# Optimization experiments

Hardware: AMD Instinct MI355X
Metric: run time of the kernel (lower is better)

## Reference

```python
import jax, jax.numpy as jnp
import numpy as np

B, G, K, C, NT = 128, 64, 32, 256, 8192


def setup_inputs() -> dict:
    key = jax.random.key(0)
    ks = jax.random.split(key, 8)
    s = lambda fan_in: 1.0 / np.sqrt(fan_in)
    return {
        "patch_features": jax.random.normal(ks[0], (B, G, C), jnp.float32),
        "neighborhood": jax.random.normal(ks[1], (B, G, K, 3), jnp.float32),
        "codebook": jax.random.normal(ks[2], (NT, C), jnp.float32),
        "w1": jax.random.normal(ks[3], (512, C), jnp.float32) * s(C),
        "b1": jnp.zeros((512,), jnp.float32),
        "w2": jax.random.normal(ks[4], (256, 512), jnp.float32) * s(512),
        "b2": jnp.zeros((256,), jnp.float32),
        "w3": jax.random.normal(ks[5], (3 * K, 256), jnp.float32) * s(256),
        "b3": jnp.zeros((3 * K,), jnp.float32),
    }


def reference(patch_features, neighborhood, codebook, w1, b1, w2, b2, w3, b3):
    b, g, c = patch_features.shape
    k = neighborhood.shape[2]
    # squared euclidean distances to codebook (argmin equals argmin of cdist p=2)
    d2 = (
        jnp.sum(patch_features * patch_features, -1, keepdims=True)
        - 2.0 * jnp.einsum("bgc,nc->bgn", patch_features, codebook)
        + jnp.sum(codebook * codebook, -1)
    )  # [B,G,NT]
    token_ids = jnp.argmin(d2, axis=-1)          # [B,G]
    quantized = codebook[token_ids]              # [B,G,C] gather
    # 1x1 Conv1d stack == per-token MLP
    h = jax.nn.relu(jnp.einsum("bgc,oc->bgo", quantized, w1) + b1)
    h = jax.nn.relu(jnp.einsum("bgc,oc->bgo", h, w2) + b2)
    rec = jnp.einsum("bgc,oc->bgo", h, w3) + b3  # [B,G,3K]
    rec = rec.reshape(b * g, k, 3)
    gt = neighborhood.reshape(b * g, k, 3)
    # Chamfer distance L2 (squared) both directions
    diff = rec[:, :, None, :] - gt[:, None, :, :]  # [BG,K,K,3]
    dd = jnp.sum(diff * diff, -1)                  # [BG,K,K]
    loss = jnp.mean(jnp.min(dd, axis=2)) + jnp.mean(jnp.min(dd, axis=1))
    return loss
```

## Files before the change

### kernel.cpp

```cpp
#include <hip/hip_runtime.h>
#include <hip/hip_bf16.h>
#include <float.h>

#define NTOK 8192
#define NCB  8192
#define CDIM 256
#define KPTS 32
#define SQNT 24.0f
#define INV_CFOLD (SQNT * SQNT * 64.0f)

typedef __attribute__((ext_vector_type(8))) short short8;
typedef __attribute__((ext_vector_type(4))) float f32x4;
typedef __attribute__((ext_vector_type(4))) int i32x4;
typedef unsigned int u32;
typedef unsigned long long u64;

__device__ __forceinline__ void gl_lds16(const void* g, void* l) {
  __builtin_amdgcn_global_load_lds(
      (const __attribute__((address_space(1))) u32*)(g),
      (__attribute__((address_space(3))) u32*)(l), 16, 0, 0);
}

__device__ __forceinline__ ushort bf16_rne(float x) {
  u32 u = __float_as_uint(x);
  return (ushort)((u + 0x7fffu + ((u >> 16) & 1u)) >> 16);
}

__device__ __forceinline__ int pack4i8(int a, int b, int c, int d) {
  return (a & 0xff) | ((b & 0xff) << 8) | ((c & 0xff) << 16) | ((d & 0xff) << 24);
}

__global__ __launch_bounds__(256) void prep_k(
    const float* __restrict__ pf, const float* __restrict__ cb,
    const float* __restrict__ w1, const float* __restrict__ w2,
    const float* __restrict__ w3,
    i32x4* __restrict__ pf1, i32x4* __restrict__ pf2,
    i32x4* __restrict__ cb1, i32x4* __restrict__ cb2,
    ushort* __restrict__ cb_bf, ushort* __restrict__ w1s,
    ushort* __restrict__ w2s, ushort* __restrict__ w3s,
    float* __restrict__ cnorm) {
  int gid = blockIdx.x * 4 + (threadIdx.x >> 6);
  int lane = threadIdx.x & 63, r16 = lane & 15, quad = lane >> 4;
  if (gid < 4096) {
    bool is_cb = gid >= 2048;
    int t = is_cb ? gid - 2048 : gid;
    int tile = t >> 2, kb = t & 3;
    const float* src = is_cb ? cb : pf;
    int row = tile * 16 + r16;
    const float* sp = src + (size_t)row * CDIM + kb * 64 + quad * 16;
    float4 v0 = ((const float4*)sp)[0];
    float4 v1 = ((const float4*)sp)[1];
    float4 v2 = ((const float4*)sp)[2];
    float4 v3 = ((const float4*)sp)[3];
    float x[16] = {v0.x, v0.y, v0.z, v0.w, v1.x, v1.y, v1.z, v1.w,
                   v2.x, v2.y, v2.z, v2.w, v3.x, v3.y, v3.z, v3.w};
    int q1[16], q2[16];
    float s = 0.f;
#pragma unroll
    for (int e = 0; e < 16; e++) {
      float as = x[e] * SQNT;
      float a1 = rintf(as);
      a1 = fminf(fmaxf(a1, -127.f), 127.f);
      float a2 = rintf((as - a1) * 128.f);
      a2 = fminf(fmaxf(a2, -127.f), 127.f);
      q1[e] = (int)a1;
      q2[e] = (int)a2;
      s += x[e] * x[e];
    }
    i32x4 p1 = {pack4i8(q1[0], q1[1], q1[2], q1[3]),
                pack4i8(q1[4], q1[5], q1[6], q1[7]),
                pack4i8(q1[8], q1[9], q1[10], q1[11]),
                pack4i8(q1[12], q1[13], q1[14], q1[15])};
    i32x4 p2 = {pack4i8(q2[0], q2[1], q2[2], q2[3]),
                pack4i8(q2[4], q2[5], q2[6], q2[7]),
                pack4i8(q2[8], q2[9], q2[10], q2[11]),
                pack4i8(q2[12], q2[13], q2[14], q2[15])};
    size_t o = (size_t)t * 64 + lane;
    (is_cb ? cb1 : pf1)[o] = p1;
    (is_cb ? cb2 : pf2)[o] = p2;
    if (is_cb) {
      s += __shfl_xor(s, 16, 64);
      s += __shfl_xor(s, 32, 64);
      if (quad == 0) atomicAdd(cnorm + row, s);
    }
  } else if (gid < 8192) {
    int t = gid - 4096;
    int tile = t >> 3, kb = t & 7;
    int row = tile * 16 + r16;
    const float* sp = cb + (size_t)row * CDIM + kb * 32 + quad * 8;
    float4 a = ((const float4*)sp)[0];
    float4 b = ((const float4*)sp)[1];
    short8 vh = {(short)bf16_rne(a.x), (short)bf16_rne(a.y),
                 (short)bf16_rne(a.z), (short)bf16_rne(a.w),
                 (short)bf16_rne(b.x), (short)bf16_rne(b.y),
                 (short)bf16_rne(b.z), (short)bf16_rne(b.w)};
    *(short8*)(cb_bf + ((size_t)tile * 8 + kb) * 512 + lane * 8) = vh;
  } else if (gid < 8752) {
    int t = gid - 8192;
    const float* src;
    ushort* dst;
    int KB;
    if (t < 256)      { src = w1; dst = w1s; KB = 8; }
    else if (t < 512) { src = w2; dst = w2s; KB = 16; t -= 256; }
    else              { src = w3; dst = w3s; KB = 8;  t -= 512; }
    int tile = t / KB, kb = t - tile * KB, K = KB * 32;
    int row = tile * 16 + r16;
    const float* sp = src + (size_t)row * K + kb * 32 + quad * 8;
    float4 a = ((const float4*)sp)[0];
    float4 b = ((const float4*)sp)[1];
    short8 vh = {(short)bf16_rne(a.x), (short)bf16_rne(a.y),
                 (short)bf16_rne(a.z), (short)bf16_rne(a.w),
                 (short)bf16_rne(b.x), (short)bf16_rne(b.y),
                 (short)bf16_rne(b.z), (short)bf16_rne(b.w)};
    *(short8*)(dst + ((size_t)tile * KB + kb) * 512 + lane * 8) = vh;
  }
}

__global__ __launch_bounds__(256, 2) void argmin_k(
    const char* __restrict__ A1g, const char* __restrict__ A2g,
    const char* __restrict__ B1g, const char* __restrict__ B2g,
    const float* __restrict__ cnorm, u64* __restrict__ pkeys) {
  __shared__ char lds[2][32768];
  int tid = threadIdx.x;
  int ns = blockIdx.x, mt = blockIdx.y;
  int wv = tid >> 6, lane = tid & 63;
  int quad = lane >> 4, r16 = lane & 15;
  int wr = wv >> 1, wc = wv & 1;

  int bvi[4][4], bii[4][4];
#pragma unroll
  for (int i = 0; i < 4; i++)
#pragma unroll
    for (int r = 0; r < 4; r++) { bvi[i][r] = 0x7fffffff; bii[i][r] = 0x7fffffff; }

  const char* bsrc = (wv == 0) ? A1g : (wv == 1) ? A2g : (wv == 2) ? B1g : B2g;

  i32x4 am[4][4], ac[4][4];

  auto stage = [&](int s) {
    int nts = s >> 2, kb = s & 3;
    int nt = ns * 4 + nts;
    char* dst = lds[s & 1] + wv * 8192;
    int gt0 = ((wv < 2) ? mt : nt) * 8;
#pragma unroll
    for (int u = 0; u < 8; ++u)
      gl_lds16(bsrc + ((size_t)(gt0 + u) * 4 + kb) * 1024 + lane * 16,
               dst + u * 1024);
  };

  stage(0);
  __syncthreads();
  for (int s = 0; s < 16; ++s) {
    int kb = s & 3, nts = s >> 2;
    if (kb == 0) {
#pragma unroll
      for (int i = 0; i < 4; i++)
#pragma unroll
        for (int j = 0; j < 4; j++) {
          am[i][j] = (i32x4){0, 0, 0, 0};
          ac[i][j] = (i32x4){0, 0, 0, 0};
        }
    }
    if (s < 15) stage(s + 1);
    const char* L = lds[s & 1];
    i32x4 f1[4], f2[4], g1[4], g2[4];
#pragma unroll
    for (int i = 0; i < 4; i++) {
      f1[i] = *(const i32x4*)(L + (wr * 4 + i) * 1024 + lane * 16);
      f2[i] = *(const i32x4*)(L + (8 + wr * 4 + i) * 1024 + lane * 16);
    }
#pragma unroll
    for (int j = 0; j < 4; j++) {
      g1[j] = *(const i32x4*)(L + (16 + wc * 4 + j) * 1024 + lane * 16);
      g2[j] = *(const i32x4*)(L + (24 + wc * 4 + j) * 1024 + lane * 16);
    }
#pragma unroll
    for (int i = 0; i < 4; i++)
#pragma unroll
      for (int j = 0; j < 4; j++) {
        am[i][j] = __builtin_amdgcn_mfma_i32_16x16x64_i8(f1[i], g1[j], am[i][j], 0, 0, 0);
        ac[i][j] = __builtin_amdgcn_mfma_i32_16x16x64_i8(f1[i], g2[j], ac[i][j], 0, 0, 0);
        ac[i][j] = __builtin_amdgcn_mfma_i32_16x16x64_i8(f2[i], g1[j], ac[i][j], 0, 0, 0);
      }
    if (kb == 3) {
      int nt = ns * 4 + nts;
#pragma unroll
      for (int j = 0; j < 4; j++) {
        int col = nt * 128 + wc * 64 + j * 16 + r16;
        int cni = __float2int_rn(cnorm[col] * INV_CFOLD);
#pragma unroll
        for (int i = 0; i < 4; i++)
#pragma unroll
          for (int r = 0; r < 4; r++) {
            int di = cni - (am[i][j][r] * 128 + ac[i][j][r]);
            if (di < bvi[i][r]) { bvi[i][r] = di; bii[i][r] = col; }
          }
      }
    }
    __syncthreads();
  }
#pragma unroll
  for (int m = 1; m < 16; m <<= 1) {
#pragma unroll
    for (int i = 0; i < 4; i++)
#pragma unroll
      for (int r = 0; r < 4; r++) {
        int ov = __shfl_xor(bvi[i][r], m, 64);
        int oi = __shfl_xor(bii[i][r], m, 64);
        if (ov < bvi[i][r] || (ov == bvi[i][r] && oi < bii[i][r])) {
          bvi[i][r] = ov;
          bii[i][r] = oi;
        }
      }
  }
  if (r16 == 0) {
#pragma unroll
    for (int i = 0; i < 4; i++)
#pragma unroll
      for (int r = 0; r < 4; r++) {
        int row = mt * 128 + wr * 64 + i * 16 + quad * 4 + r;
        u32 mk = (u32)(bvi[i][r] + (1 << 30));
        pkeys[(size_t)(ns * 2 + wc) * NTOK + row] = ((u64)mk << 32) | (u32)bii[i][r];
      }
  }
}

__global__ __launch_bounds__(512) void mlp_fused_k(
    const u64* __restrict__ pkeys, const ushort* __restrict__ cb_bf,
    const ushort* __restrict__ w1s, const float* __restrict__ b1,
    const ushort* __restrict__ w2s, const float* __restrict__ b2,
    const ushort* __restrict__ w3s, const float* __restrict__ b3,
    const float* __restrict__ neigh, float* __restrict__ out) {
  __shared__ ushort qs_h2[8 * 512];
  __shared__ ushort h1s[16 * 512];
  __shared__ float rec[16 * 96];
  __shared__ float gts[16 * 96];
  __shared__ int ids[16];
  __shared__ float wsum[8];

  int tid = threadIdx.x;
  int t0 = blockIdx.x * 16;
  int wv = tid >> 6, lane = tid & 63;
  int quad = lane >> 4, r16 = lane & 15;

  {
    int row_l = tid >> 5, sl = tid & 31;
    u64 best = pkeys[(size_t)sl * NTOK + t0 + row_l];
#pragma unroll
    for (int m = 1; m < 32; m <<= 1) {
      u64 o = __shfl_xor((unsigned long long)best, m, 64);
      if (o < best) best = o;
    }
    if (sl == 0) ids[row_l] = (int)(u32)best;
  }
  __syncthreads();

  {
    int kb = wv;
    int id = ids[r16];
    short8 v = *(const short8*)(cb_bf + ((size_t)(id >> 4) * 8 + kb) * 512 +
                                (size_t)((id & 15) + quad * 16) * 8);
    *(short8*)(qs_h2 + (size_t)kb * 512 + lane * 8) = v;
  }
  __syncthreads();

  short8 fa1[8];
#pragma unroll
  for (int kb = 0; kb < 8; kb++)
    fa1[kb] = *(const short8*)(qs_h2 + (size_t)kb * 512 + lane * 8);
  __syncthreads();

#pragma unroll
  for (int jj = 0; jj < 4; ++jj) {
    int jt = wv + jj * 8;
    f32x4 acc = (f32x4){0.f, 0.f, 0.f, 0.f};
#pragma unroll
    for (int kb = 0; kb < 8; kb++) {
      short8 fb = *(const short8*)(w1s + ((size_t)jt * 8 + kb) * 512 + lane * 8);
      acc = __builtin_amdgcn_mfma_f32_16x16x32_bf16(fa1[kb], fb, acc, 0, 0, 0);
    }
    int col = jt * 16 + r16;
    float bj = b1[col];
#pragma unroll
    for (int reg = 0; reg < 4; reg++) {
      int row_l = quad * 4 + reg;
      float v = fmaxf(acc[reg] + bj, 0.f);
      size_t o = (size_t)(col >> 5) * 512 +
                 (size_t)(((col >> 3) & 3) * 16 + row_l) * 8 + (col & 7);
      h1s[o] = bf16_rne(v);
    }
  }
  __syncthreads();

#pragma unroll
  for (int jj = 0; jj < 2; ++jj) {
    int jt = wv + jj * 8;
    f32x4 acc = (f32x4){0.f, 0.f, 0.f, 0.f};
#pragma unroll
    for (int kb = 0; kb < 16; kb++) {
      short8 fa = *(const short8*)(h1s + (size_t)kb * 512 + lane * 8);
      short8 fb = *(const short8*)(w2s + ((size_t)jt * 16 + kb) * 512 + lane * 8);
      acc = __builtin_amdgcn_mfma_f32_16x16x32_bf16(fa, fb, acc, 0, 0, 0);
    }
    int col = jt * 16 + r16;
    float bj = b2[col];
#pragma unroll
    for (int reg = 0; reg < 4; reg++) {
      int row_l = quad * 4 + reg;
      float v = fmaxf(acc[reg] + bj, 0.f);
      size_t o = (size_t)(col >> 5) * 512 +
                 (size_t)(((col >> 3) & 3) * 16 + row_l) * 8 + (col & 7);
      qs_h2[o] = bf16_rne(v);
    }
  }
  __syncthreads();

  if (tid < 384) {
    int t = tid / 24, c = (tid - t * 24) * 4;
    *(float4*)(gts + (size_t)t * 96 + c) =
        *(const float4*)(neigh + (size_t)(t0 + t) * 96 + c);
  }

  if (wv < 6) {
    int jt = wv;
    f32x4 acc = (f32x4){0.f, 0.f, 0.f, 0.f};
#pragma unroll
    for (int kb = 0; kb < 8; kb++) {
      short8 fa = *(const short8*)(qs_h2 + (size_t)kb * 512 + lane * 8);
      short8 fb = *(const short8*)(w3s + ((size_t)jt * 8 + kb) * 512 + lane * 8);
      acc = __builtin_amdgcn_mfma_f32_16x16x32_bf16(fa, fb, acc, 0, 0, 0);
    }
    int col = jt * 16 + r16;
    float bj = b3[col];
#pragma unroll
    for (int reg = 0; reg < 4; reg++) {
      int row_l = quad * 4 + reg;
      rec[(size_t)row_l * 96 + col] = acc[reg] + bj;
    }
  }
  __syncthreads();

  float local = 0.f;
  {
    int t = tid >> 5, i = tid & 31;
    float rx = rec[t * 96 + 3 * i], ry = rec[t * 96 + 3 * i + 1], rz = rec[t * 96 + 3 * i + 2];
    float gx = gts[t * 96 + 3 * i], gy = gts[t * 96 + 3 * i + 1], gz = gts[t * 96 + 3 * i + 2];
    float mA = FLT_MAX, mB = FLT_MAX;
#pragma unroll
    for (int j = 0; j < 32; j++) {
      float dx = rx - gts[t * 96 + 3 * j], dy = ry - gts[t * 96 + 3 * j + 1],
            dz = rz - gts[t * 96 + 3 * j + 2];
      float d = dx * dx + dy * dy + dz * dz;
      mA = fminf(mA, d);
      dx = rec[t * 96 + 3 * j] - gx; dy = rec[t * 96 + 3 * j + 1] - gy;
      dz = rec[t * 96 + 3 * j + 2] - gz;
      d = dx * dx + dy * dy + dz * dz;
      mB = fminf(mB, d);
    }
    local = mA + mB;
  }
#pragma unroll
  for (int off = 32; off; off >>= 1) local += __shfl_down(local, off, 64);
  if (lane == 0) wsum[wv] = local;
  __syncthreads();
  if (tid == 0) {
    float s = 0.f;
#pragma unroll
    for (int w = 0; w < 8; w++) s += wsum[w];
    atomicAdd(out, s * (1.0f / (float)(NTOK * KPTS)));
  }
}

extern "C" void kernel_launch(void* const* d_in, const int* in_sizes, int n_in,
                              void* d_out, int out_size, void* d_ws, size_t ws_size,
                              hipStream_t stream) {
  const float* pf    = (const float*)d_in[0];
  const float* neigh = (const float*)d_in[1];
  const float* cb    = (const float*)d_in[2];
  const float* w1    = (const float*)d_in[3];
  const float* b1    = (const float*)d_in[4];
  const float* w2    = (const float*)d_in[5];
  const float* b2    = (const float*)d_in[6];
  const float* w3    = (const float*)d_in[7];
  const float* b3    = (const float*)d_in[8];
  float* out = (float*)d_out;
  char* base = (char*)d_ws;

  u64*   pkeys = (u64*)base;
  float* cnorm = (float*)(base + 0x200000);
  char*  pf1   = base + 0x210000;
  char*  pf2   = base + 0x410000;
  char*  cb1   = base + 0x610000;
  char*  cb2   = base + 0x810000;
  ushort* cb_bf = (ushort*)(base + 0xA10000);
  ushort* w1s   = (ushort*)(base + 0xE10000);
  ushort* w2s   = (ushort*)(base + 0xE50000);
  ushort* w3s   = (ushort*)(base + 0xE90000);

  hipMemsetAsync(d_out, 0, sizeof(float), stream);
  hipMemsetAsync(cnorm, 0, NCB * sizeof(float), stream);
  prep_k<<<2188, 256, 0, stream>>>(pf, cb, w1, w2, w3,
                                   (i32x4*)pf1, (i32x4*)pf2, (i32x4*)cb1,
                                   (i32x4*)cb2, cb_bf, w1s, w2s, w3s, cnorm);
  argmin_k<<<dim3(16, 64), 256, 0, stream>>>(pf1, pf2, cb1, cb2, cnorm, pkeys);
  mlp_fused_k<<<512, 512, 0, stream>>>(pkeys, cb_bf, w1s, b1, w2s, b2,
                                       w3s, b3, neigh, out);
}
```

Measured before the change: 167.0 us.

## Retile argmin and MLP kernels, fuse codebook bf16 conversion and norm reduction

Prep now writes the bf16 codebook from the same loads used for int8 quantization and reduces codebook norms in shared memory instead of with atomics, which drops a memset and about half the prep blocks. The argmin kernel shrinks its M tile to 64 rows, uses a single 24KB LDS buffer and targets 3 blocks per CU. This trades the double-buffered prefetch for more occupancy and smaller register footprint. The MLP kernel processes 32 tokens per block so each weight fragment load feeds two MFMAs.

```diff
diff --git a/kernel.cpp b/kernel.cpp
--- a/kernel.cpp
+++ b/kernel.cpp
@@ -39,7 +39,9 @@
     ushort* __restrict__ cb_bf, ushort* __restrict__ w1s,
     ushort* __restrict__ w2s, ushort* __restrict__ w3s,
     float* __restrict__ cnorm) {
+  __shared__ float cred[4][16];
   int gid = blockIdx.x * 4 + (threadIdx.x >> 6);
+  int wv = threadIdx.x >> 6;
   int lane = threadIdx.x & 63, r16 = lane & 15, quad = lane >> 4;
   if (gid < 4096) {
     bool is_cb = gid >= 2048;
@@ -79,24 +81,33 @@
     (is_cb ? cb1 : pf1)[o] = p1;
     (is_cb ? cb2 : pf2)[o] = p2;
     if (is_cb) {
+      int kb32 = 2 * kb + (quad >> 1);
+      int slot0 = ((2 * quad) & 3) * 16 + r16;
+      int slot1 = ((2 * quad + 1) & 3) * 16 + r16;
+      size_t bo = ((size_t)tile * 8 + kb32) * 512;
+      short8 vh0 = {(short)bf16_rne(x[0]), (short)bf16_rne(x[1]),
+                    (short)bf16_rne(x[2]), (short)bf16_rne(x[3]),
+                    (short)bf16_rne(x[4]), (short)bf16_rne(x[5]),
+                    (short)bf16_rne(x[6]), (short)bf16_rne(x[7])};
+      short8 vh1 = {(short)bf16_rne(x[8]), (short)bf16_rne(x[9]),
+                    (short)bf16_rne(x[10]), (short)bf16_rne(x[11]),
+                    (short)bf16_rne(x[12]), (short)bf16_rne(x[13]),
+                    (short)bf16_rne(x[14]), (short)bf16_rne(x[15])};
+      *(short8*)(cb_bf + bo + (size_t)slot0 * 8) = vh0;
+      *(short8*)(cb_bf + bo + (size_t)slot1 * 8) = vh1;
       s += __shfl_xor(s, 16, 64);
       s += __shfl_xor(s, 32, 64);
-      if (quad == 0) atomicAdd(cnorm + row, s);
-    }
-  } else if (gid < 8192) {
+      if (quad == 0) cred[wv][r16] = s;
+      __syncthreads();
+      if (threadIdx.x < 16) {
+        int ctile = blockIdx.x - 512;
+        cnorm[ctile * 16 + threadIdx.x] =
+            cred[0][threadIdx.x] + cred[1][threadIdx.x] +
+            cred[2][threadIdx.x] + cred[3][threadIdx.x];
+      }
+    }
+  } else if (gid < 4656) {
     int t = gid - 4096;
-    int tile = t >> 3, kb = t & 7;
-    int row = tile * 16 + r16;
-    const float* sp = cb + (size_t)row * CDIM + kb * 32 + quad * 8;
-    float4 a = ((const float4*)sp)[0];
-    float4 b = ((const float4*)sp)[1];
-    short8 vh = {(short)bf16_rne(a.x), (short)bf16_rne(a.y),
-                 (short)bf16_rne(a.z), (short)bf16_rne(a.w),
-                 (short)bf16_rne(b.x), (short)bf16_rne(b.y),
-                 (short)bf16_rne(b.z), (short)bf16_rne(b.w)};
-    *(short8*)(cb_bf + ((size_t)tile * 8 + kb) * 512 + lane * 8) = vh;
-  } else if (gid < 8752) {
-    int t = gid - 8192;
     const float* src;
     ushort* dst;
     int KB;
@@ -116,80 +127,73 @@
   }
 }
 
-__global__ __launch_bounds__(256, 2) void argmin_k(
+__global__ __launch_bounds__(256, 3) void argmin_k(
     const char* __restrict__ A1g, const char* __restrict__ A2g,
     const char* __restrict__ B1g, const char* __restrict__ B2g,
     const float* __restrict__ cnorm, u64* __restrict__ pkeys) {
-  __shared__ char lds[2][32768];
+  __shared__ char lds[24 * 1024];
   int tid = threadIdx.x;
   int ns = blockIdx.x, mt = blockIdx.y;
   int wv = tid >> 6, lane = tid & 63;
   int quad = lane >> 4, r16 = lane & 15;
   int wr = wv >> 1, wc = wv & 1;
 
-  int bvi[4][4], bii[4][4];
-#pragma unroll
-  for (int i = 0; i < 4; i++)
+  int bvi[2][4], bii[2][4];
+#pragma unroll
+  for (int i = 0; i < 2; i++)
 #pragma unroll
     for (int r = 0; r < 4; r++) { bvi[i][r] = 0x7fffffff; bii[i][r] = 0x7fffffff; }
 
-  const char* bsrc = (wv == 0) ? A1g : (wv == 1) ? A2g : (wv == 2) ? B1g : B2g;
-
-  i32x4 am[4][4], ac[4][4];
-
-  auto stage = [&](int s) {
+  i32x4 am[2][4], ac[2][4];
+
+  for (int s = 0; s < 16; ++s) {
     int nts = s >> 2, kb = s & 3;
     int nt = ns * 4 + nts;
-    char* dst = lds[s & 1] + wv * 8192;
-    int gt0 = ((wv < 2) ? mt : nt) * 8;
-#pragma unroll
-    for (int u = 0; u < 8; ++u)
-      gl_lds16(bsrc + ((size_t)(gt0 + u) * 4 + kb) * 1024 + lane * 16,
-               dst + u * 1024);
-  };
-
-  stage(0);
-  __syncthreads();
-  for (int s = 0; s < 16; ++s) {
-    int kb = s & 3, nts = s >> 2;
+#pragma unroll
+    for (int u = 0; u < 6; ++u) {
+      int c = wv + u * 4;
+      const char* src;
+      int gt;
+      if (c < 4)       { src = A1g; gt = mt * 4 + c; }
+      else if (c < 8)  { src = A2g; gt = mt * 4 + (c - 4); }
+      else if (c < 16) { src = B1g; gt = nt * 8 + (c - 8); }
+      else             { src = B2g; gt = nt * 8 + (c - 16); }
+      gl_lds16(src + ((size_t)gt * 4 + kb) * 1024 + lane * 16, lds + c * 1024);
+    }
+    __syncthreads();
     if (kb == 0) {
 #pragma unroll
-      for (int i = 0; i < 4; i++)
+      for (int i = 0; i < 2; i++)
 #pragma unroll
         for (int j = 0; j < 4; j++) {
           am[i][j] = (i32x4){0, 0, 0, 0};
           ac[i][j] = (i32x4){0, 0, 0, 0};
         }
     }
-    if (s < 15) stage(s + 1);
-    const char* L = lds[s & 1];
-    i32x4 f1[4], f2[4], g1[4], g2[4];
-#pragma unroll
-    for (int i = 0; i < 4; i++) {
-      f1[i] = *(const i32x4*)(L + (wr * 4 + i) * 1024 + lane * 16);
-      f2[i] = *(const i32x4*)(L + (8 + wr * 4 + i) * 1024 + lane * 16);
+    i32x4 f1[2], f2[2];
+#pragma unroll
+    for (int i = 0; i < 2; i++) {
+      f1[i] = *(const i32x4*)(lds + (wr * 2 + i) * 1024 + lane * 16);
+      f2[i] = *(const i32x4*)(lds + 4096 + (wr * 2 + i) * 1024 + lane * 16);
     }
 #pragma unroll
     for (int j = 0; j < 4; j++) {
-      g1[j] = *(const i32x4*)(L + (16 + wc * 4 + j) * 1024 + lane * 16);
-      g2[j] = *(const i32x4*)(L + (24 + wc * 4 + j) * 1024 + lane * 16);
-    }
-#pragma unroll
-    for (int i = 0; i < 4; i++)
-#pragma unroll
-      for (int j = 0; j < 4; j++) {
-        am[i][j] = __builtin_amdgcn_mfma_i32_16x16x64_i8(f1[i], g1[j], am[i][j], 0, 0, 0);
-        ac[i][j] = __builtin_amdgcn_mfma_i32_16x16x64_i8(f1[i], g2[j], ac[i][j], 0, 0, 0);
-        ac[i][j] = __builtin_amdgcn_mfma_i32_16x16x64_i8(f2[i], g1[j], ac[i][j], 0, 0, 0);
-      }
+      i32x4 g1 = *(const i32x4*)(lds + 8192 + (wc * 4 + j) * 1024 + lane * 16);
+      i32x4 g2 = *(const i32x4*)(lds + 16384 + (wc * 4 + j) * 1024 + lane * 16);
+#pragma unroll
+      for (int i = 0; i < 2; i++) {
+        am[i][j] = __builtin_amdgcn_mfma_i32_16x16x64_i8(f1[i], g1, am[i][j], 0, 0, 0);
+        ac[i][j] = __builtin_amdgcn_mfma_i32_16x16x64_i8(f1[i], g2, ac[i][j], 0, 0, 0);
+        ac[i][j] = __builtin_amdgcn_mfma_i32_16x16x64_i8(f2[i], g1, ac[i][j], 0, 0, 0);
+      }
+    }
     if (kb == 3) {
-      int nt = ns * 4 + nts;
 #pragma unroll
       for (int j = 0; j < 4; j++) {
         int col = nt * 128 + wc * 64 + j * 16 + r16;
         int cni = __float2int_rn(cnorm[col] * INV_CFOLD);
 #pragma unroll
-        for (int i = 0; i < 4; i++)
+        for (int i = 0; i < 2; i++)
 #pragma unroll
           for (int r = 0; r < 4; r++) {
             int di = cni - (am[i][j][r] * 128 + ac[i][j][r]);
@@ -202,7 +206,7 @@
 #pragma unroll
   for (int m = 1; m < 16; m <<= 1) {
 #pragma unroll
-    for (int i = 0; i < 4; i++)
+    for (int i = 0; i < 2; i++)
 #pragma unroll
       for (int r = 0; r < 4; r++) {
         int ov = __shfl_xor(bvi[i][r], m, 64);
@@ -215,10 +219,10 @@
   }
   if (r16 == 0) {
 #pragma unroll
-    for (int i = 0; i < 4; i++)
+    for (int i = 0; i < 2; i++)
 #pragma unroll
       for (int r = 0; r < 4; r++) {
-        int row = mt * 128 + wr * 64 + i * 16 + quad * 4 + r;
+        int row = mt * 64 + wr * 32 + i * 16 + quad * 4 + r;
         u32 mk = (u32)(bvi[i][r] + (1 << 30));
         pkeys[(size_t)(ns * 2 + wc) * NTOK + row] = ((u64)mk << 32) | (u32)bii[i][r];
       }
@@ -231,23 +235,26 @@
     const ushort* __restrict__ w2s, const float* __restrict__ b2,
     const ushort* __restrict__ w3s, const float* __restrict__ b3,
     const float* __restrict__ neigh, float* __restrict__ out) {
-  __shared__ ushort qs_h2[8 * 512];
-  __shared__ ushort h1s[16 * 512];
-  __shared__ float rec[16 * 96];
-  __shared__ float gts[16 * 96];
-  __shared__ int ids[16];
-  __shared__ float wsum[8];
+  extern __shared__ char lds[];
+  ushort* qsp = (ushort*)lds;
+  ushort* h1p = (ushort*)(lds + 16384);
+  float* recp = (float*)(lds + 16384);
+  float* gtsp = (float*)(lds + 28672);
+  int* ids = (int*)(lds + 49152);
+  float* wsum = (float*)(lds + 49280);
 
   int tid = threadIdx.x;
-  int t0 = blockIdx.x * 16;
+  int t0 = blockIdx.x * 32;
   int wv = tid >> 6, lane = tid & 63;
   int quad = lane >> 4, r16 = lane & 15;
 
   {
-    int row_l = tid >> 5, sl = tid & 31;
-    u64 best = pkeys[(size_t)sl * NTOK + t0 + row_l];
-#pragma unroll
-    for (int m = 1; m < 32; m <<= 1) {
+    int row_l = tid >> 4, sl = tid & 15;
+    u64 a = pkeys[(size_t)sl * NTOK + t0 + row_l];
+    u64 b = pkeys[(size_t)(sl + 16) * NTOK + t0 + row_l];
+    u64 best = a < b ? a : b;
+#pragma unroll
+    for (int m = 1; m < 16; m <<= 1) {
       u64 o = __shfl_xor((unsigned long long)best, m, 64);
       if (o < best) best = o;
     }
@@ -255,39 +262,46 @@
   }
   __syncthreads();
 
-  {
-    int kb = wv;
-    int id = ids[r16];
-    short8 v = *(const short8*)(cb_bf + ((size_t)(id >> 4) * 8 + kb) * 512 +
+#pragma unroll
+  for (int t = 0; t < 2; t++) {
+    int id = ids[t * 16 + r16];
+    short8 v = *(const short8*)(cb_bf + ((size_t)(id >> 4) * 8 + wv) * 512 +
                                 (size_t)((id & 15) + quad * 16) * 8);
-    *(short8*)(qs_h2 + (size_t)kb * 512 + lane * 8) = v;
-  }
-  __syncthreads();
-
-  short8 fa1[8];
-#pragma unroll
-  for (int kb = 0; kb < 8; kb++)
-    fa1[kb] = *(const short8*)(qs_h2 + (size_t)kb * 512 + lane * 8);
-  __syncthreads();
+    *(short8*)(qsp + (size_t)(t * 8 + wv) * 512 + lane * 8) = v;
+  }
+  __syncthreads();
+
+  short8 fa1[2][8];
+#pragma unroll
+  for (int t = 0; t < 2; t++)
+#pragma unroll
+    for (int kb = 0; kb < 8; kb++)
+      fa1[t][kb] = *(const short8*)(qsp + (size_t)(t * 8 + kb) * 512 + lane * 8);
 
 #pragma unroll
   for (int jj = 0; jj < 4; ++jj) {
     int jt = wv + jj * 8;
-    f32x4 acc = (f32x4){0.f, 0.f, 0.f, 0.f};
+    f32x4 acc0 = (f32x4){0.f, 0.f, 0.f, 0.f};
+    f32x4 acc1 = (f32x4){0.f, 0.f, 0.f, 0.f};
 #pragma unroll
     for (int kb = 0; kb < 8; kb++) {
       short8 fb = *(const short8*)(w1s + ((size_t)jt * 8 + kb) * 512 + lane * 8);
-      acc = __builtin_amdgcn_mfma_f32_16x16x32_bf16(fa1[kb], fb, acc, 0, 0, 0);
+      acc0 = __builtin_amdgcn_mfma_f32_16x16x32_bf16(fa1[0][kb], fb, acc0, 0, 0, 0);
+      acc1 = __builtin_amdgcn_mfma_f32_16x16x32_bf16(fa1[1][kb], fb, acc1, 0, 0, 0);
     }
     int col = jt * 16 + r16;
     float bj = b1[col];
 #pragma unroll
-    for (int reg = 0; reg < 4; reg++) {
-      int row_l = quad * 4 + reg;
-      float v = fmaxf(acc[reg] + bj, 0.f);
-      size_t o = (size_t)(col >> 5) * 512 +
-                 (size_t)(((col >> 3) & 3) * 16 + row_l) * 8 + (col & 7);
-      h1s[o] = bf16_rne(v);
+    for (int t = 0; t < 2; t++) {
+      f32x4 acc = t ? acc1 : acc0;
+#pragma unroll
+      for (int reg = 0; reg < 4; reg++) {
+        int row_l = quad * 4 + reg;
+        float v = fmaxf(acc[reg] + bj, 0.f);
+        size_t o = (size_t)(t * 16 + (col >> 5)) * 512 +
+                   (size_t)(((col >> 3) & 3) * 16 + row_l) * 8 + (col & 7);
+        h1p[o] = bf16_rne(v);
+      }
     }
   }
   __syncthreads();
@@ -295,69 +309,89 @@
 #pragma unroll
   for (int jj = 0; jj < 2; ++jj) {
     int jt = wv + jj * 8;
-    f32x4 acc = (f32x4){0.f, 0.f, 0.f, 0.f};
+    f32x4 acc0 = (f32x4){0.f, 0.f, 0.f, 0.f};
+    f32x4 acc1 = (f32x4){0.f, 0.f, 0.f, 0.f};
 #pragma unroll
     for (int kb = 0; kb < 16; kb++) {
-      short8 fa = *(const short8*)(h1s + (size_t)kb * 512 + lane * 8);
       short8 fb = *(const short8*)(w2s + ((size_t)jt * 16 + kb) * 512 + lane * 8);
-      acc = __builtin_amdgcn_mfma_f32_16x16x32_bf16(fa, fb, acc, 0, 0, 0);
+      short8 fa0 = *(const short8*)(h1p + (size_t)kb * 512 + lane * 8);
+      short8 fa1v = *(const short8*)(h1p + (size_t)(16 + kb) * 512 + lane * 8);
+      acc0 = __builtin_amdgcn_mfma_f32_16x16x32_bf16(fa0, fb, acc0, 0, 0, 0);
+      acc1 = __builtin_amdgcn_mfma_f32_16x16x32_bf16(fa1v, fb, acc1, 0, 0, 0);
     }
     int col = jt * 16 + r16;
     float bj = b2[col];
 #pragma unroll
-    for (int reg = 0; reg < 4; reg++) {
-      int row_l = quad * 4 + reg;
-      float v = fmaxf(acc[reg] + bj, 0.f);
-      size_t o = (size_t)(col >> 5) * 512 +
-                 (size_t)(((col >> 3) & 3) * 16 + row_l) * 8 + (col & 7);
-      qs_h2[o] = bf16_rne(v);
-    }
-  }
-  __syncthreads();
-
-  if (tid < 384) {
-    int t = tid / 24, c = (tid - t * 24) * 4;
-    *(float4*)(gts + (size_t)t * 96 + c) =
-        *(const float4*)(neigh + (size_t)(t0 + t) * 96 + c);
+    for (int t = 0; t < 2; t++) {
+      f32x4 acc = t ? acc1 : acc0;
+#pragma unroll
+      for (int reg = 0; reg < 4; reg++) {
+        int row_l = quad * 4 + reg;
+        float v = fmaxf(acc[reg] + bj, 0.f);
+        size_t o = (size_t)(t * 8 + (col >> 5)) * 512 +
+                   (size_t)(((col >> 3) & 3) * 16 + row_l) * 8 + (col & 7);
+        qsp[o] = bf16_rne(v);
+      }
+    }
+  }
+  __syncthreads();
+
+#pragma unroll
+  for (int s = 0; s < 2; s++) {
+    int idx = tid + s * 512;
+    if (idx < 768) {
+      int t = idx / 24, c = (idx - t * 24) * 4;
+      *(float4*)(gtsp + (size_t)t * 96 + c) =
+          *(const float4*)(neigh + (size_t)(t0 + t) * 96 + c);
+    }
   }
 
   if (wv < 6) {
     int jt = wv;
-    f32x4 acc = (f32x4){0.f, 0.f, 0.f, 0.f};
+    f32x4 acc0 = (f32x4){0.f, 0.f, 0.f, 0.f};
+    f32x4 acc1 = (f32x4){0.f, 0.f, 0.f, 0.f};
 #pragma unroll
     for (int kb = 0; kb < 8; kb++) {
-      short8 fa = *(const short8*)(qs_h2 + (size_t)kb * 512 + lane * 8);
       short8 fb = *(const short8*)(w3s + ((size_t)jt * 8 + kb) * 512 + lane * 8);
-      acc = __builtin_amdgcn_mfma_f32_16x16x32_bf16(fa, fb, acc, 0, 0, 0);
+      short8 fa0 = *(const short8*)(qsp + (size_t)kb * 512 + lane * 8);
+      short8 fa1v = *(const short8*)(qsp + (size_t)(8 + kb) * 512 + lane * 8);
+      acc0 = __builtin_amdgcn_mfma_f32_16x16x32_bf16(fa0, fb, acc0, 0, 0, 0);
+      acc1 = __builtin_amdgcn_mfma_f32_16x16x32_bf16(fa1v, fb, acc1, 0, 0, 0);
     }
     int col = jt * 16 + r16;
     float bj = b3[col];
 #pragma unroll
-    for (int reg = 0; reg < 4; reg++) {
-      int row_l = quad * 4 + reg;
-      rec[(size_t)row_l * 96 + col] = acc[reg] + bj;
+    for (int t = 0; t < 2; t++) {
+      f32x4 acc = t ? acc1 : acc0;
+#pragma unroll
+      for (int reg = 0; reg < 4; reg++) {
+        int row_l = quad * 4 + reg;
+        recp[(size_t)(t * 16 + row_l) * 96 + col] = acc[reg] + bj;
+      }
     }
   }
   __syncthreads();
 
   float local = 0.f;
-  {
-    int t = tid >> 5, i = tid & 31;
-    float rx = rec[t * 96 + 3 * i], ry = rec[t * 96 + 3 * i + 1], rz = rec[t * 96 + 3 * i + 2];
-    float gx = gts[t * 96 + 3 * i], gy = gts[t * 96 + 3 * i + 1], gz = gts[t * 96 + 3 * i + 2];
+#pragma unroll
+  for (int pp = 0; pp < 2; ++pp) {
+    int p = tid + pp * 512;
+    int t = p >> 5, i = p & 31;
+    float rx = recp[t * 96 + 3 * i], ry = recp[t * 96 + 3 * i + 1], rz = recp[t * 96 + 3 * i + 2];
+    float gx = gtsp[t * 96 + 3 * i], gy = gtsp[t * 96 + 3 * i + 1], gz = gtsp[t * 96 + 3 * i + 2];
     float mA = FLT_MAX, mB = FLT_MAX;
 #pragma unroll
     for (int j = 0; j < 32; j++) {
-      float dx = rx - gts[t * 96 + 3 * j], dy = ry - gts[t * 96 + 3 * j + 1],
-            dz = rz - gts[t * 96 + 3 * j + 2];
+      float dx = rx - gtsp[t * 96 + 3 * j], dy = ry - gtsp[t * 96 + 3 * j + 1],
+            dz = rz - gtsp[t * 96 + 3 * j + 2];
       float d = dx * dx + dy * dy + dz * dz;
       mA = fminf(mA, d);
-      dx = rec[t * 96 + 3 * j] - gx; dy = rec[t * 96 + 3 * j + 1] - gy;
-      dz = rec[t * 96 + 3 * j + 2] - gz;
+      dx = recp[t * 96 + 3 * j] - gx; dy = recp[t * 96 + 3 * j + 1] - gy;
+      dz = recp[t * 96 + 3 * j + 2] - gz;
       d = dx * dx + dy * dy + dz * dz;
       mB = fminf(mB, d);
     }
-    local = mA + mB;
+    local += mA + mB;
   }
 #pragma unroll
   for (int off = 32; off; off >>= 1) local += __shfl_down(local, off, 64);
@@ -398,11 +432,10 @@
   ushort* w3s   = (ushort*)(base + 0xE90000);
 
   hipMemsetAsync(d_out, 0, sizeof(float), stream);
-  hipMemsetAsync(cnorm, 0, NCB * sizeof(float), stream);
-  prep_k<<<2188, 256, 0, stream>>>(pf, cb, w1, w2, w3,
+  prep_k<<<1164, 256, 0, stream>>>(pf, cb, w1, w2, w3,
                                    (i32x4*)pf1, (i32x4*)pf2, (i32x4*)cb1,
                                    (i32x4*)cb2, cb_bf, w1s, w2s, w3s, cnorm);
-  argmin_k<<<dim3(16, 64), 256, 0, stream>>>(pf1, pf2, cb1, cb2, cnorm, pkeys);
-  mlp_fused_k<<<512, 512, 0, stream>>>(pkeys, cb_bf, w1s, b1, w2s, b2,
-                                       w3s, b3, neigh, out);
-}
+  argmin_k<<<dim3(16, 128), 256, 0, stream>>>(pf1, pf2, cb1, cb2, cnorm, pkeys);
+  mlp_fused_k<<<256, 512, 49344, stream>>>(pkeys, cb_bf, w1s, b1, w2s, b2,
+                                           w3s, b3, neigh, out);
+}
```

Measured after the change: 171.6 us. 2.8% more time.

## Keep argmin A tiles resident in LDS and fuse codebook bf16 conversion into prep

Applied to the files above, without the earlier changes.

The argmin kernel now loads the full int8 feature tile (both quantization planes, all K blocks) into 64KB of dynamic LDS once and streams only codebook tiles per step. This removes repeated A-tile reloads but drops the previous double-buffered prefetch, so codebook loads are no longer overlapped with MFMA work. The prep kernel converts the codebook to bf16 in the same pass that produces the int8 planes, which avoids a second read of the codebook. It also writes codebook norms with a per-block LDS reduction instead of atomics and zeroes the output in-kernel, which removes both memsets.

```diff
diff --git a/kernel.cpp b/kernel.cpp
--- a/kernel.cpp
+++ b/kernel.cpp
@@ -38,8 +38,11 @@
     i32x4* __restrict__ cb1, i32x4* __restrict__ cb2,
     ushort* __restrict__ cb_bf, ushort* __restrict__ w1s,
     ushort* __restrict__ w2s, ushort* __restrict__ w3s,
-    float* __restrict__ cnorm) {
+    float* __restrict__ cnorm, float* __restrict__ out) {
+  __shared__ float cred[4][16];
+  if (blockIdx.x == 0 && threadIdx.x == 0) out[0] = 0.f;
   int gid = blockIdx.x * 4 + (threadIdx.x >> 6);
+  int wv = threadIdx.x >> 6;
   int lane = threadIdx.x & 63, r16 = lane & 15, quad = lane >> 4;
   if (gid < 4096) {
     bool is_cb = gid >= 2048;
@@ -79,24 +82,33 @@
     (is_cb ? cb1 : pf1)[o] = p1;
     (is_cb ? cb2 : pf2)[o] = p2;
     if (is_cb) {
+      int kb32 = 2 * kb + (quad >> 1);
+      int slot0 = ((2 * quad) & 3) * 16 + r16;
+      int slot1 = ((2 * quad + 1) & 3) * 16 + r16;
+      size_t bo = ((size_t)tile * 8 + kb32) * 512;
+      short8 vh0 = {(short)bf16_rne(x[0]), (short)bf16_rne(x[1]),
+                    (short)bf16_rne(x[2]), (short)bf16_rne(x[3]),
+                    (short)bf16_rne(x[4]), (short)bf16_rne(x[5]),
+                    (short)bf16_rne(x[6]), (short)bf16_rne(x[7])};
+      short8 vh1 = {(short)bf16_rne(x[8]), (short)bf16_rne(x[9]),
+                    (short)bf16_rne(x[10]), (short)bf16_rne(x[11]),
+                    (short)bf16_rne(x[12]), (short)bf16_rne(x[13]),
+                    (short)bf16_rne(x[14]), (short)bf16_rne(x[15])};
+      *(short8*)(cb_bf + bo + (size_t)slot0 * 8) = vh0;
+      *(short8*)(cb_bf + bo + (size_t)slot1 * 8) = vh1;
       s += __shfl_xor(s, 16, 64);
       s += __shfl_xor(s, 32, 64);
-      if (quad == 0) atomicAdd(cnorm + row, s);
-    }
-  } else if (gid < 8192) {
+      if (quad == 0) cred[wv][r16] = s;
+      __syncthreads();
+      if (threadIdx.x < 16) {
+        int ctile = blockIdx.x - 512;
+        cnorm[ctile * 16 + threadIdx.x] =
+            cred[0][threadIdx.x] + cred[1][threadIdx.x] +
+            cred[2][threadIdx.x] + cred[3][threadIdx.x];
+      }
+    }
+  } else if (gid < 4656) {
     int t = gid - 4096;
-    int tile = t >> 3, kb = t & 7;
-    int row = tile * 16 + r16;
-    const float* sp = cb + (size_t)row * CDIM + kb * 32 + quad * 8;
-    float4 a = ((const float4*)sp)[0];
-    float4 b = ((const float4*)sp)[1];
-    short8 vh = {(short)bf16_rne(a.x), (short)bf16_rne(a.y),
-                 (short)bf16_rne(a.z), (short)bf16_rne(a.w),
-                 (short)bf16_rne(b.x), (short)bf16_rne(b.y),
-                 (short)bf16_rne(b.z), (short)bf16_rne(b.w)};
-    *(short8*)(cb_bf + ((size_t)tile * 8 + kb) * 512 + lane * 8) = vh;
-  } else if (gid < 8752) {
-    int t = gid - 8192;
     const float* src;
     ushort* dst;
     int KB;
@@ -120,7 +132,10 @@
     const char* __restrict__ A1g, const char* __restrict__ A2g,
     const char* __restrict__ B1g, const char* __restrict__ B2g,
     const float* __restrict__ cnorm, u64* __restrict__ pkeys) {
-  __shared__ char lds[2][32768];
+  extern __shared__ char lds[];
+  char* A1 = lds;
+  char* A2 = lds + 32768;
+  char* Bb = lds + 65536;
   int tid = threadIdx.x;
   int ns = blockIdx.x, mt = blockIdx.y;
   int wv = tid >> 6, lane = tid & 63;
@@ -133,25 +148,28 @@
 #pragma unroll
     for (int r = 0; r < 4; r++) { bvi[i][r] = 0x7fffffff; bii[i][r] = 0x7fffffff; }
 
-  const char* bsrc = (wv == 0) ? A1g : (wv == 1) ? A2g : (wv == 2) ? B1g : B2g;
+#pragma unroll
+  for (int u = 0; u < 16; ++u) {
+    int c = wv + u * 4;
+    const char* src = (c < 32) ? A1g : A2g;
+    char* dst = (c < 32) ? A1 : A2;
+    int cc = c & 31;
+    gl_lds16(src + ((size_t)(mt * 8 + (cc >> 2)) * 4 + (cc & 3)) * 1024 + lane * 16,
+             dst + cc * 1024);
+  }
 
   i32x4 am[4][4], ac[4][4];
-
-  auto stage = [&](int s) {
+  for (int s = 0; s < 16; ++s) {
     int nts = s >> 2, kb = s & 3;
     int nt = ns * 4 + nts;
-    char* dst = lds[s & 1] + wv * 8192;
-    int gt0 = ((wv < 2) ? mt : nt) * 8;
-#pragma unroll
-    for (int u = 0; u < 8; ++u)
-      gl_lds16(bsrc + ((size_t)(gt0 + u) * 4 + kb) * 1024 + lane * 16,
-               dst + u * 1024);
-  };
-
-  stage(0);
-  __syncthreads();
-  for (int s = 0; s < 16; ++s) {
-    int kb = s & 3, nts = s >> 2;
+#pragma unroll
+    for (int u = 0; u < 4; ++u) {
+      int c = wv * 4 + u;
+      const char* src = (c < 8) ? B1g : B2g;
+      int gt = nt * 8 + (c & 7);
+      gl_lds16(src + ((size_t)gt * 4 + kb) * 1024 + lane * 16, Bb + c * 1024);
+    }
+    __syncthreads();
     if (kb == 0) {
 #pragma unroll
       for (int i = 0; i < 4; i++)
@@ -161,18 +179,16 @@
           ac[i][j] = (i32x4){0, 0, 0, 0};
         }
     }
-    if (s < 15) stage(s + 1);
-    const char* L = lds[s & 1];
     i32x4 f1[4], f2[4], g1[4], g2[4];
 #pragma unroll
     for (int i = 0; i < 4; i++) {
-      f1[i] = *(const i32x4*)(L + (wr * 4 + i) * 1024 + lane * 16);
-      f2[i] = *(const i32x4*)(L + (8 + wr * 4 + i) * 1024 + lane * 16);
+      f1[i] = *(const i32x4*)(A1 + ((wr * 4 + i) * 4 + kb) * 1024 + lane * 16);
+      f2[i] = *(const i32x4*)(A2 + ((wr * 4 + i) * 4 + kb) * 1024 + lane * 16);
     }
 #pragma unroll
     for (int j = 0; j < 4; j++) {
-      g1[j] = *(const i32x4*)(L + (16 + wc * 4 + j) * 1024 + lane * 16);
-      g2[j] = *(const i32x4*)(L + (24 + wc * 4 + j) * 1024 + lane * 16);
+      g1[j] = *(const i32x4*)(Bb + (wc * 4 + j) * 1024 + lane * 16);
+      g2[j] = *(const i32x4*)(Bb + (8 + wc * 4 + j) * 1024 + lane * 16);
     }
 #pragma unroll
     for (int i = 0; i < 4; i++)
@@ -183,7 +199,6 @@
         ac[i][j] = __builtin_amdgcn_mfma_i32_16x16x64_i8(f2[i], g1[j], ac[i][j], 0, 0, 0);
       }
     if (kb == 3) {
-      int nt = ns * 4 + nts;
 #pragma unroll
       for (int j = 0; j < 4; j++) {
         int col = nt * 128 + wc * 64 + j * 16 + r16;
@@ -397,12 +412,10 @@
   ushort* w2s   = (ushort*)(base + 0xE50000);
   ushort* w3s   = (ushort*)(base + 0xE90000);
 
-  hipMemsetAsync(d_out, 0, sizeof(float), stream);
-  hipMemsetAsync(cnorm, 0, NCB * sizeof(float), stream);
-  prep_k<<<2188, 256, 0, stream>>>(pf, cb, w1, w2, w3,
+  prep_k<<<1164, 256, 0, stream>>>(pf, cb, w1, w2, w3,
                                    (i32x4*)pf1, (i32x4*)pf2, (i32x4*)cb1,
-                                   (i32x4*)cb2, cb_bf, w1s, w2s, w3s, cnorm);
-  argmin_k<<<dim3(16, 64), 256, 0, stream>>>(pf1, pf2, cb1, cb2, cnorm, pkeys);
+                                   (i32x4*)cb2, cb_bf, w1s, w2s, w3s, cnorm, out);
+  argmin_k<<<dim3(16, 64), 256, 81920, stream>>>(pf1, pf2, cb1, cb2, cnorm, pkeys);
   mlp_fused_k<<<512, 512, 0, stream>>>(pkeys, cb_bf, w1s, b1, w2s, b2,
                                        w3s, b3, neigh, out);
 }
```

Result: faster. 157.7 us (-5.5%).
